# Performance work log

Measured on AMD Instinct MI355X. Metric: run time of the kernel, lower is better.

The kernel has to match this reference:

```python
import jax, jax.numpy as jnp
import numpy as np

K = 5          # reassembly kernel size
S = 2          # scale factor
ENC_PAD = 1    # encoder_kernel_size // 2


def _conv2d(x, w, pad):
    return jax.lax.conv_general_dilated(
        x, w, window_strides=(1, 1), padding=[(pad, pad), (pad, pad)],
        dimension_numbers=('NCHW', 'OIHW', 'NCHW'))


def setup_inputs() -> dict:
    key = jax.random.key(0)
    k1, k2, k3 = jax.random.split(key, 3)
    x = jax.random.normal(k1, (2, 256, 40, 40), dtype=jnp.float32)
    # channel compressor: xavier-uniform-ish 1x1 conv weight (64, 256, 1, 1)
    limit = np.sqrt(6.0 / (256 + 64)).astype(np.float32)
    w_comp = jax.random.uniform(k2, (64, 256, 1, 1), dtype=jnp.float32,
                                minval=-limit, maxval=limit)
    # content encoder: normal(0, 0.001), out = k^2*s^2 = 100 channels
    w_enc = 0.001 * jax.random.normal(k3, (100, 64, 3, 3), dtype=jnp.float32)
    return {"x": x, "w_comp": w_comp, "w_enc": w_enc}


def reference(x, w_comp, w_enc):
    b, c, h, w = x.shape
    k2 = K * K
    h_up, w_up = h * S, w * S

    # --- kernel prediction ---
    compressed = _conv2d(x, w_comp, 0)                # (b, 64, h, w)
    kern = _conv2d(compressed, w_enc, ENC_PAD)        # (b, k2*S^2, h, w)
    # pixel shuffle: (b, k2, S, S, h, w) -> (b, k2, h, S, w, S) -> (b, k2, h_up, w_up)
    kern = kern.reshape(b, k2, S, S, h, w).transpose(0, 1, 4, 2, 5, 3)
    kern = kern.reshape(b, k2, h_up * w_up)
    kern = jax.nn.softmax(kern, axis=1)               # softmax over k2

    # --- unfold (im2col, padding K//2) ---
    pad = K // 2
    xp = jnp.pad(x, ((0, 0), (0, 0), (pad, pad), (pad, pad)))
    # (b, c, k2, h, w): channel-major, kernel offsets inner (matches torch F.unfold)
    patches = jnp.stack([xp[:, :, i:i + h, j:j + w]
                         for i in range(K) for j in range(K)], axis=2)
    x_unfold = patches.reshape(b, c, k2, h * w)

    # --- reassembly (faithful to the torch 'efficient' path) ---
    # torch repeat_interleaves x_unfold S^2 times along the h*w axis and
    # multiplies with kernels flattened in (h_up*w_up) row-major order; that
    # pairing is exactly kern reshaped to (b, k2, h*w, S^2):
    kern4 = kern.reshape(b, k2, h * w, S * S)
    out = jnp.einsum('bckp,bkpd->bcpd', x_unfold, kern4)  # (b, c, h*w, S^2)
    return out.reshape(b, c, h_up, w_up)
```

## Files before the change

kernel.cpp:

```cpp
#include <hip/hip_runtime.h>

#define B   2
#define C   256
#define CM  64
#define CE  100
#define H   40
#define W   40
#define HW  1600
#define KK  25

__global__ __launch_bounds__(256) void k1_conv1x1(
    const float* __restrict__ x, const float* __restrict__ w,
    float* __restrict__ pc) {
  const int t = blockIdx.x, ich = blockIdx.y, b = blockIdx.z;
  __shared__ __align__(16) float xs[64 * 64];
  __shared__ __align__(16) float wsA[64 * 64];
  const int tid = threadIdx.x;

  const float4* x4 = (const float4*)(x + ((size_t)b * C + ich * 64) * HW + t * 64);
#pragma unroll
  for (int i = 0; i < 4; i++) {
    int idx = tid + i * 256;
    ((float4*)xs)[idx] = x4[(idx >> 4) * 400 + (idx & 15)];
  }
  const float4* w4 = (const float4*)w;
#pragma unroll
  for (int i = 0; i < 4; i++) {
    int idx = tid + i * 256;
    int icq = idx >> 6, oc = idx & 63;
    float4 f = w4[oc * 64 + ich * 16 + icq];
    wsA[(icq * 4 + 0) * 64 + oc] = f.x;
    wsA[(icq * 4 + 1) * 64 + oc] = f.y;
    wsA[(icq * 4 + 2) * 64 + oc] = f.z;
    wsA[(icq * 4 + 3) * 64 + oc] = f.w;
  }
  __syncthreads();

  const int ty = tid >> 4, tx = tid & 15;
  float acc[4][4];
#pragma unroll
  for (int i = 0; i < 4; i++)
#pragma unroll
    for (int j = 0; j < 4; j++) acc[i][j] = 0.f;

#pragma unroll 4
  for (int icl = 0; icl < 64; icl++) {
    float4 a = *(const float4*)&wsA[icl * 64 + ty * 4];
    float4 bb = *(const float4*)&xs[icl * 64 + tx * 4];
    float av[4] = {a.x, a.y, a.z, a.w};
    float bv[4] = {bb.x, bb.y, bb.z, bb.w};
#pragma unroll
    for (int i = 0; i < 4; i++)
#pragma unroll
      for (int j = 0; j < 4; j++) acc[i][j] += av[i] * bv[j];
  }

  float* o = pc + ((size_t)ich * B + b) * CM * HW + t * 64 + tx * 4;
#pragma unroll
  for (int j = 0; j < 4; j++)
    *(float4*)&o[(size_t)(ty * 4 + j) * HW] =
        make_float4(acc[j][0], acc[j][1], acc[j][2], acc[j][3]);
}

__global__ __launch_bounds__(256) void k2_conv3x3(
    const float* __restrict__ pc, const float* __restrict__ w,
    float* __restrict__ encP) {
  const int tile = blockIdx.x, ocq = blockIdx.y, icq = blockIdx.z;
  const int ty5 = tile / 5, tx5 = tile % 5;
  __shared__ __align__(16) float smem[3200 + 16 * 9 * 28];
  float* cs  = smem;
  float* wsb = smem + 3200;
  float* pacc = smem;
  const int tid = threadIdx.x;

  for (int i = tid; i < 3200; i += 256) {
    int bb = i / 1600, r = i - bb * 1600;
    int icl = r / 100, rr = r - icl * 100;
    int yy = rr / 10, xx = rr - yy * 10;
    int gy = ty5 * 8 + yy - 1, gx = tx5 * 8 + xx - 1;
    float v = 0.f;
    if (gy >= 0 && gy < H && gx >= 0 && gx < W) {
      int o = bb * 102400 + (icq * 16 + icl) * HW + gy * W + gx;
      v = pc[o] + pc[204800 + o] + pc[409600 + o] + pc[614400 + o];
    }
    cs[i] = v;
  }
  const float* wb = w + (size_t)(ocq * 25) * 576 + (size_t)(icq * 16) * 9;
  for (int i = tid; i < 3600; i += 256) {
    int ol = i / 144, r = i - ol * 144;
    wsb[r * 28 + ol] = wb[ol * 576 + r];
  }
  __syncthreads();

  const int wv = tid >> 6, lane = tid & 63, py = lane >> 3, px = lane & 7;
  float acc[50];
#pragma unroll
  for (int j = 0; j < 50; j++) acc[j] = 0.f;

#pragma unroll 1
  for (int t = 0; t < 4; t++) {
    const int icl = wv * 4 + t;
    const float* c0 = &cs[icl * 100 + py * 10 + px];
    const float* c1 = c0 + 1600;
    const float* wrow = &wsb[icl * 9 * 28];
#pragma unroll
    for (int dy = 0; dy < 3; dy++) {
#pragma unroll
      for (int dx = 0; dx < 3; dx++) {
        float x0 = c0[dy * 10 + dx];
        float x1 = c1[dy * 10 + dx];
        const float* wp = &wrow[(dy * 3 + dx) * 28];
        float4 w0 = *(const float4*)&wp[0],  w1 = *(const float4*)&wp[4];
        float4 w2 = *(const float4*)&wp[8],  w3 = *(const float4*)&wp[12];
        float4 w4v = *(const float4*)&wp[16], w5 = *(const float4*)&wp[20];
        float w6 = wp[24];
        acc[0]  += x0 * w0.x;  acc[1]  += x0 * w0.y;  acc[2]  += x0 * w0.z;  acc[3]  += x0 * w0.w;
        acc[4]  += x0 * w1.x;  acc[5]  += x0 * w1.y;  acc[6]  += x0 * w1.z;  acc[7]  += x0 * w1.w;
        acc[8]  += x0 * w2.x;  acc[9]  += x0 * w2.y;  acc[10] += x0 * w2.z;  acc[11] += x0 * w2.w;
        acc[12] += x0 * w3.x;  acc[13] += x0 * w3.y;  acc[14] += x0 * w3.z;  acc[15] += x0 * w3.w;
        acc[16] += x0 * w4v.x; acc[17] += x0 * w4v.y; acc[18] += x0 * w4v.z; acc[19] += x0 * w4v.w;
        acc[20] += x0 * w5.x;  acc[21] += x0 * w5.y;  acc[22] += x0 * w5.z;  acc[23] += x0 * w5.w;
        acc[24] += x0 * w6;
        acc[25] += x1 * w0.x;  acc[26] += x1 * w0.y;  acc[27] += x1 * w0.z;  acc[28] += x1 * w0.w;
        acc[29] += x1 * w1.x;  acc[30] += x1 * w1.y;  acc[31] += x1 * w1.z;  acc[32] += x1 * w1.w;
        acc[33] += x1 * w2.x;  acc[34] += x1 * w2.y;  acc[35] += x1 * w2.z;  acc[36] += x1 * w2.w;
        acc[37] += x1 * w3.x;  acc[38] += x1 * w3.y;  acc[39] += x1 * w3.z;  acc[40] += x1 * w3.w;
        acc[41] += x1 * w4v.x; acc[42] += x1 * w4v.y; acc[43] += x1 * w4v.z; acc[44] += x1 * w4v.w;
        acc[45] += x1 * w5.x;  acc[46] += x1 * w5.y;  acc[47] += x1 * w5.z;  acc[48] += x1 * w5.w;
        acc[49] += x1 * w6;
      }
    }
  }

  __syncthreads();
  if (wv == 1 || wv == 3) {
    const int slot = wv >> 1;
#pragma unroll
    for (int j = 0; j < 50; j++) pacc[slot * 3200 + j * 64 + lane] = acc[j];
  }
  __syncthreads();
  if (wv == 0 || wv == 2) {
    const int slot = wv >> 1;
#pragma unroll
    for (int j = 0; j < 50; j++) acc[j] += pacc[slot * 3200 + j * 64 + lane];
  }
  __syncthreads();
  if (wv == 2) {
#pragma unroll
    for (int j = 0; j < 50; j++) pacc[j * 64 + lane] = acc[j];
  }
  __syncthreads();
  if (wv == 0) {
    const int base_px = (ty5 * 8 + py) * W + tx5 * 8 + px;
#pragma unroll
    for (int bb = 0; bb < 2; bb++)
#pragma unroll
      for (int ol = 0; ol < 25; ol++)
        encP[(((size_t)icq * 2 + bb) * CE + ocq * 25 + ol) * HW + base_px] =
            acc[bb * 25 + ol] + pacc[(bb * 25 + ol) * 64 + lane];
  }
}

__global__ __launch_bounds__(256) void k3_reassemble(
    const float* __restrict__ x, const float* __restrict__ encP,
    float* __restrict__ out) {
  const int i0 = blockIdx.x >> 1;
  const int jh = blockIdx.x & 1;
  const int cq = blockIdx.y;
  const int b = blockIdx.z;

  __shared__ __align__(16) float wlds[20 * KK * 4];
  __shared__ float xsm[64 * 121];

  const int tid = threadIdx.x;

  if (tid < 80) {
    const int e = jh * 80 + tid;
    const int j0 = e >> 2, d = e & 3;
    const int off = ((e >= 80) ? 2 : 0) + (e & 1);
    const int col = ((e >= 80) ? (j0 - 20) : j0) * 2 + (d >> 1);
    const float* ep = encP + (size_t)b * CE * HW + i0 * W + col;
    float v[KK];
    float m = -1e30f;
#pragma unroll
    for (int k = 0; k < KK; k++) {
      int o = (k * 4 + off) * HW;
      v[k] = ep[o] + ep[320000 + o] + ep[640000 + o] + ep[960000 + o];
      m = fmaxf(m, v[k]);
    }
    float s = 0.f;
#pragma unroll
    for (int k = 0; k < KK; k++) {
      v[k] = expf(v[k] - m);
      s += v[k];
    }
    const float inv = 1.f / s;
    const int j0l = j0 - jh * 20;
#pragma unroll
    for (int k = 0; k < KK; k++) wlds[(j0l * KK + k) * 4 + d] = v[k] * inv;
  }

  const float* xb = x + ((size_t)b * C + cq * 64) * HW;
  for (int i = tid; i < 64 * 120; i += 256) {
    int c = i / 120;
    int rr = i % 120;
    int r = rr / 24, t = rr % 24;
    int gy = i0 - 2 + r;
    int gx = jh * 20 + t - 2;
    float v = 0.f;
    if (gy >= 0 && gy < H && gx >= 0 && gx < W) v = xb[c * HW + gy * W + gx];
    xsm[c * 121 + r * 24 + t] = v;
  }
  __syncthreads();

  const int wv = tid >> 6;
  const int lane = tid & 63;
  const int j0b = wv * 5;
  const float* xrow = &xsm[lane * 121];
  float* ob = out + (((size_t)b * C + cq * 64 + lane) * 6400) + i0 * 160;

  float a[5][4];
#pragma unroll
  for (int jj = 0; jj < 5; jj++)
#pragma unroll
    for (int d = 0; d < 4; d++) a[jj][d] = 0.f;

#pragma unroll
  for (int ki = 0; ki < 5; ki++) {
    float xv[9];
    const float* xr = &xrow[ki * 24 + j0b];
#pragma unroll
    for (int q = 0; q < 9; q++) xv[q] = xr[q];
    const float* wrow = &wlds[(j0b * KK + ki * 5) * 4];
#pragma unroll
    for (int jj = 0; jj < 5; jj++) {
#pragma unroll
      for (int kj = 0; kj < 5; kj++) {
        float4 w4 = *(const float4*)&wrow[(jj * KK + kj) * 4];
        float xvv = xv[jj + kj];
        a[jj][0] += xvv * w4.x;
        a[jj][1] += xvv * w4.y;
        a[jj][2] += xvv * w4.z;
        a[jj][3] += xvv * w4.w;
      }
    }
  }
#pragma unroll
  for (int jj = 0; jj < 5; jj++)
    *(float4*)&ob[(jh * 20 + j0b + jj) * 4] =
        make_float4(a[jj][0], a[jj][1], a[jj][2], a[jj][3]);
}

extern "C" void kernel_launch(void* const* d_in, const int* in_sizes, int n_in,
                              void* d_out, int out_size, void* d_ws, size_t ws_size,
                              hipStream_t stream) {
  const float* x      = (const float*)d_in[0];
  const float* w_comp = (const float*)d_in[1];
  const float* w_enc  = (const float*)d_in[2];
  float* out = (float*)d_out;

  float* pc   = (float*)d_ws;
  float* encP = (float*)((char*)d_ws + 3276800);

  k1_conv1x1<<<dim3(25, 4, B), 256, 0, stream>>>(x, w_comp, pc);
  k2_conv3x3<<<dim3(25, 4, 4), 256, 0, stream>>>(pc, w_enc, encP);
  k3_reassemble<<<dim3(80, 4, B), 256, 0, stream>>>(x, encP, out);
}
```

Before: 110.6 us.

## Fuse three stages into one cooperative persistent kernel with grid syncs

Merges the 1x1 conv, 3x3 conv and reassembly kernels into a single cooperative kernel of 256 blocks. Each block loops over the work units of every stage, and grid-wide syncs with thread fences separate the stages. This removes two kernel launch boundaries and their tail gaps. In exchange, stages B and C run fewer blocks than before, so some blocks do two work units while others idle. The host also queries device attributes and occupancy on every call, and falls back to the original three launches if cooperative launch is not supported.

```diff
diff --git a/kernel.cpp b/kernel.cpp
--- a/kernel.cpp
+++ b/kernel.cpp
@@ -1,4 +1,7 @@
 #include <hip/hip_runtime.h>
+#include <hip/hip_cooperative_groups.h>
+
+namespace cg = cooperative_groups;
 
 #define B   2
 #define C   256
@@ -9,13 +12,14 @@
 #define HW  1600
 #define KK  25
 
-__global__ __launch_bounds__(256) void k1_conv1x1(
-    const float* __restrict__ x, const float* __restrict__ w,
+
+__device__ __forceinline__ void stageA_body(
+    int u, int tid, float* smem,
+    const float* __restrict__ x, const float* __restrict__ wc,
     float* __restrict__ pc) {
-  const int t = blockIdx.x, ich = blockIdx.y, b = blockIdx.z;
-  __shared__ __align__(16) float xs[64 * 64];
-  __shared__ __align__(16) float wsA[64 * 64];
-  const int tid = threadIdx.x;
+  const int t = u % 25, ich = (u / 25) % 4, b = u / 100;
+  float* xs  = smem;
+  float* wsA = smem + 4096;
 
   const float4* x4 = (const float4*)(x + ((size_t)b * C + ich * 64) * HW + t * 64);
 #pragma unroll
@@ -23,7 +27,7 @@
     int idx = tid + i * 256;
     ((float4*)xs)[idx] = x4[(idx >> 4) * 400 + (idx & 15)];
   }
-  const float4* w4 = (const float4*)w;
+  const float4* w4 = (const float4*)wc;
 #pragma unroll
   for (int i = 0; i < 4; i++) {
     int idx = tid + i * 256;
@@ -62,16 +66,15 @@
         make_float4(acc[j][0], acc[j][1], acc[j][2], acc[j][3]);
 }
 
-__global__ __launch_bounds__(256) void k2_conv3x3(
-    const float* __restrict__ pc, const float* __restrict__ w,
+__device__ __forceinline__ void stageB_body(
+    int u, int tid, float* smem,
+    const float* __restrict__ pc, const float* __restrict__ we,
     float* __restrict__ encP) {
-  const int tile = blockIdx.x, ocq = blockIdx.y, icq = blockIdx.z;
+  const int tile = u % 25, ocq = (u / 25) % 4, icq = u / 100;
   const int ty5 = tile / 5, tx5 = tile % 5;
-  __shared__ __align__(16) float smem[3200 + 16 * 9 * 28];
-  float* cs  = smem;
-  float* wsb = smem + 3200;
+  float* cs   = smem;
+  float* wsb  = smem + 3200;
   float* pacc = smem;
-  const int tid = threadIdx.x;
 
   for (int i = tid; i < 3200; i += 256) {
     int bb = i / 1600, r = i - bb * 1600;
@@ -85,7 +88,7 @@
     }
     cs[i] = v;
   }
-  const float* wb = w + (size_t)(ocq * 25) * 576 + (size_t)(icq * 16) * 9;
+  const float* wb = we + (size_t)(ocq * 25) * 576 + (size_t)(icq * 16) * 9;
   for (int i = tid; i < 3600; i += 256) {
     int ol = i / 144, r = i - ol * 144;
     wsb[r * 28 + ol] = wb[ol * 576 + r];
@@ -161,18 +164,17 @@
   }
 }
 
-__global__ __launch_bounds__(256) void k3_reassemble(
+__device__ __forceinline__ void stageC_body(
+    int u, int tid, float* smem,
     const float* __restrict__ x, const float* __restrict__ encP,
     float* __restrict__ out) {
-  const int i0 = blockIdx.x >> 1;
-  const int jh = blockIdx.x & 1;
-  const int cq = blockIdx.y;
-  const int b = blockIdx.z;
-
-  __shared__ __align__(16) float wlds[20 * KK * 4];
-  __shared__ float xsm[64 * 121];
-
-  const int tid = threadIdx.x;
+  const int bx = u % 80;
+  const int i0 = bx >> 1;
+  const int jh = bx & 1;
+  const int cq = (u / 80) % 4;
+  const int b = u / 320;
+  float* wlds = smem;
+  float* xsm  = smem + 2000;
 
   if (tid < 80) {
     const int e = jh * 80 + tid;
@@ -251,6 +253,54 @@
         make_float4(a[jj][0], a[jj][1], a[jj][2], a[jj][3]);
 }
 
+__global__ __launch_bounds__(256) void k_fused(
+    const float* __restrict__ x, const float* __restrict__ wc,
+    const float* __restrict__ we, float* __restrict__ pc,
+    float* __restrict__ encP, float* __restrict__ out) {
+  __shared__ __align__(16) float smem[9744];
+  const int tid = threadIdx.x;
+  const int bid = blockIdx.x;
+  cg::grid_group grid = cg::this_grid();
+
+  if (bid < 200) stageA_body(bid, tid, smem, x, wc, pc);
+  __syncthreads();
+  __threadfence();
+  grid.sync();
+
+  for (int u = bid; u < 400; u += 256) {
+    stageB_body(u, tid, smem, pc, we, encP);
+    __syncthreads();
+  }
+  __threadfence();
+  grid.sync();
+
+  for (int u = bid; u < 640; u += 256) {
+    stageC_body(u, tid, smem, x, encP, out);
+    __syncthreads();
+  }
+}
+
+__global__ __launch_bounds__(256) void k1_conv1x1(
+    const float* __restrict__ x, const float* __restrict__ w,
+    float* __restrict__ pc) {
+  __shared__ __align__(16) float smem[8192];
+  stageA_body(blockIdx.x, threadIdx.x, smem, x, w, pc);
+}
+
+__global__ __launch_bounds__(256) void k2_conv3x3(
+    const float* __restrict__ pc, const float* __restrict__ w,
+    float* __restrict__ encP) {
+  __shared__ __align__(16) float smem[7232];
+  stageB_body(blockIdx.x, threadIdx.x, smem, pc, w, encP);
+}
+
+__global__ __launch_bounds__(256) void k3_reassemble(
+    const float* __restrict__ x, const float* __restrict__ encP,
+    float* __restrict__ out) {
+  __shared__ __align__(16) float smem[9744];
+  stageC_body(blockIdx.x, threadIdx.x, smem, x, encP, out);
+}
+
 extern "C" void kernel_launch(void* const* d_in, const int* in_sizes, int n_in,
                               void* d_out, int out_size, void* d_ws, size_t ws_size,
                               hipStream_t stream) {
@@ -262,7 +312,19 @@
   float* pc   = (float*)d_ws;
   float* encP = (float*)((char*)d_ws + 3276800);
 
-  k1_conv1x1<<<dim3(25, 4, B), 256, 0, stream>>>(x, w_comp, pc);
-  k2_conv3x3<<<dim3(25, 4, 4), 256, 0, stream>>>(pc, w_enc, encP);
-  k3_reassemble<<<dim3(80, 4, B), 256, 0, stream>>>(x, encP, out);
-}
+  int coop = 0, ncu = 0, maxb = 0;
+  hipDeviceGetAttribute(&coop, hipDeviceAttributeCooperativeLaunch, 0);
+  hipDeviceGetAttribute(&ncu, hipDeviceAttributeMultiprocessorCount, 0);
+  hipOccupancyMaxActiveBlocksPerMultiprocessor(&maxb, k_fused, 256, 0);
+
+  if (coop && (long)ncu * maxb >= 256) {
+    void* args[] = {(void*)&x, (void*)&w_comp, (void*)&w_enc,
+                    (void*)&pc, (void*)&encP, (void*)&out};
+    hipLaunchCooperativeKernel(reinterpret_cast<void*>(k_fused),
+                               dim3(256), dim3(256), args, 0, stream);
+  } else {
+    k1_conv1x1<<<dim3(200), 256, 0, stream>>>(x, w_comp, pc);
+    k2_conv3x3<<<dim3(400), 256, 0, stream>>>(pc, w_enc, encP);
+    k3_reassemble<<<dim3(640), 256, 0, stream>>>(x, encP, out);
+  }
+}
```

Result: slower. 278.8 us (+152.2%).
